# Kernel tuning notes

Measured on AMD Instinct MI355X. Metric: run time of the kernel, lower is better.

## Reference

```python
import jax, jax.numpy as jnp
import numpy as np

NODE, EDGE, GLOB, HID = 128, 64, 64, 32
E, B = 500000, 1024
IN = 2 * NODE + EDGE + GLOB  # 384


def setup_inputs() -> dict:
    key = jax.random.key(0)
    ks = jax.random.split(key, 9)
    src = jax.random.normal(ks[0], (E, NODE), dtype=jnp.float32)
    dest = jax.random.normal(ks[1], (E, NODE), dtype=jnp.float32)
    edge_attr = jax.random.normal(ks[2], (E, EDGE), dtype=jnp.float32)
    u = jax.random.normal(ks[3], (B, GLOB), dtype=jnp.float32)
    batch = jnp.sort(jax.random.randint(ks[4], (E,), 0, B, dtype=jnp.int64))
    # MLP params (Linear stores weight [out,in]; we keep [in,out] for x@W)
    s1 = 1.0 / np.sqrt(IN)
    s2 = 1.0 / np.sqrt(HID)
    W1 = jax.random.uniform(ks[5], (IN, HID), jnp.float32, -s1, s1)
    b1 = jax.random.uniform(ks[6], (HID,), jnp.float32, -s1, s1)
    W2 = jax.random.uniform(ks[7], (HID, EDGE), jnp.float32, -s2, s2)
    b2 = jax.random.uniform(ks[8], (EDGE,), jnp.float32, -s2, s2)
    return {"src": src, "dest": dest, "edge_attr": edge_attr, "u": u,
            "batch": batch, "W1": W1, "b1": b1, "W2": W2, "b2": b2}


def reference(src, dest, edge_attr, u, batch, W1, b1, W2, b2):
    # gather per-edge global features, concat, 2-layer MLP with SELU
    x = jnp.concatenate([src, dest, edge_attr, u[batch]], axis=1)  # [E, 384]
    h = jax.nn.selu(x @ W1 + b1)  # [E, 32]
    return h @ W2 + b2            # [E, 64]
```

## Files before the change

### kernel.cpp

```cpp
#include <hip/hip_runtime.h>
#include <hip/hip_bf16.h>

#define N_E    500000
#define D_NODE 128
#define D_EDGE 64
#define D_GLOB 64
#define NTILES (N_E / 16)

typedef __attribute__((ext_vector_type(8))) short s16x8;
typedef __attribute__((ext_vector_type(4))) float fx4;

__device__ __forceinline__ unsigned short f2bf(float x) {
  union { __hip_bfloat16 h; unsigned short u; } cv;
  cv.h = __float2bfloat16(x);
  return cv.u;
}

__device__ __forceinline__ s16x8 pack8(fx4 a, fx4 b) {
  s16x8 r;
  r[0] = (short)f2bf(a[0]); r[1] = (short)f2bf(a[1]);
  r[2] = (short)f2bf(a[2]); r[3] = (short)f2bf(a[3]);
  r[4] = (short)f2bf(b[0]); r[5] = (short)f2bf(b[1]);
  r[6] = (short)f2bf(b[2]); r[7] = (short)f2bf(b[3]);
  return r;
}

__global__ __launch_bounds__(256) void edge_mlp_kernel(
    const float* __restrict__ src, const float* __restrict__ dst,
    const float* __restrict__ ea,  const float* __restrict__ u,
    const int*   __restrict__ batch,
    const float* __restrict__ W1,  const float* __restrict__ b1,
    const float* __restrict__ W2,  const float* __restrict__ b2,
    float* __restrict__ out)
{
  __shared__ unsigned short w1t[32][392];
  __shared__ unsigned short w2t[64][40];
  __shared__ float b1s[32];
  __shared__ float b2s[64];
  __shared__ unsigned short hstage[4][16][40];

  const int tid = threadIdx.x;

  for (int i = tid; i < 384 * 32; i += 256) {
    int k = i >> 5, n = i & 31;
    w1t[n][k] = f2bf(W1[i]);
  }
  for (int i = tid; i < 32 * 64; i += 256) {
    int k = i >> 6, n = i & 63;
    w2t[n][k] = f2bf(W2[i]);
  }
  if (tid < 32) b1s[tid] = b1[tid];
  if (tid < 64) b2s[tid] = b2[tid];
  __syncthreads();

  const int wave = tid >> 6;
  const int lane = tid & 63;
  const int c  = lane & 15;
  const int r4 = lane >> 4;
  const int r8 = r4 * 8;
  unsigned short (*hl)[40] = hstage[wave];

  const int gwave  = blockIdx.x * 4 + wave;
  const int nwaves = gridDim.x * 4;

  const float lam = 1.0507009873554805f;
  const float la  = 1.7580993408473766f;

  for (int tile = gwave; tile < NTILES; tile += nwaves) {
    const int e0   = tile * 16;
    const int arow = e0 + c;

    const float* sp  = src + (size_t)arow * D_NODE + r8;
    const float* dp  = dst + (size_t)arow * D_NODE + r8;
    const float* epp = ea  + (size_t)arow * D_EDGE + r8;
    const int    bt  = batch[arow];
    const float* up  = u   + (size_t)bt * D_GLOB + r8;

    const float* bases[12] = { sp, sp + 32, sp + 64, sp + 96,
                               dp, dp + 32, dp + 64, dp + 96,
                               epp, epp + 32, up, up + 32 };
    fx4 raw[24];
#pragma unroll
    for (int i = 0; i < 12; ++i) {
      const fx4* q = (const fx4*)bases[i];
      raw[2 * i]     = q[0];
      raw[2 * i + 1] = q[1];
    }

    s16x8 af[12];
#pragma unroll
    for (int i = 0; i < 12; ++i) af[i] = pack8(raw[2 * i], raw[2 * i + 1]);

    fx4 acc0 = {0.f, 0.f, 0.f, 0.f};
    fx4 acc1 = {0.f, 0.f, 0.f, 0.f};
#pragma unroll
    for (int kk = 0; kk < 12; ++kk) {
      s16x8 bf0 = *(const s16x8*)&w1t[c][kk * 32 + r8];
      s16x8 bf1 = *(const s16x8*)&w1t[c + 16][kk * 32 + r8];
      acc0 = __builtin_amdgcn_mfma_f32_16x16x32_bf16(af[kk], bf0, acc0, 0, 0, 0);
      acc1 = __builtin_amdgcn_mfma_f32_16x16x32_bf16(af[kk], bf1, acc1, 0, 0, 0);
    }

#pragma unroll
    for (int t = 0; t < 2; ++t) {
      const float bb = b1s[c + 16 * t];
      fx4 a = t ? acc1 : acc0;
#pragma unroll
      for (int r = 0; r < 4; ++r) {
        float v = a[r] + bb;
        v = v > 0.f ? lam * v : la * (__expf(v) - 1.f);
        hl[r4 * 4 + r][c + 16 * t] = f2bf(v);
      }
    }

    s16x8 a2 = *(const s16x8*)&hl[c][r8];
    fx4 o0, o1, o2, o3;
    { float bb = b2s[c];      o0 = (fx4){bb, bb, bb, bb}; }
    { float bb = b2s[c + 16]; o1 = (fx4){bb, bb, bb, bb}; }
    { float bb = b2s[c + 32]; o2 = (fx4){bb, bb, bb, bb}; }
    { float bb = b2s[c + 48]; o3 = (fx4){bb, bb, bb, bb}; }
    o0 = __builtin_amdgcn_mfma_f32_16x16x32_bf16(a2, *(const s16x8*)&w2t[c][r8],      o0, 0, 0, 0);
    o1 = __builtin_amdgcn_mfma_f32_16x16x32_bf16(a2, *(const s16x8*)&w2t[c + 16][r8], o1, 0, 0, 0);
    o2 = __builtin_amdgcn_mfma_f32_16x16x32_bf16(a2, *(const s16x8*)&w2t[c + 32][r8], o2, 0, 0, 0);
    o3 = __builtin_amdgcn_mfma_f32_16x16x32_bf16(a2, *(const s16x8*)&w2t[c + 48][r8], o3, 0, 0, 0);

#pragma unroll
    for (int r = 0; r < 4; ++r) {
      float* op = out + (size_t)(e0 + r4 * 4 + r) * 64 + c;
      op[0]  = o0[r];
      op[16] = o1[r];
      op[32] = o2[r];
      op[48] = o3[r];
    }
  }
}

extern "C" void kernel_launch(void* const* d_in, const int* in_sizes, int n_in,
                              void* d_out, int out_size, void* d_ws, size_t ws_size,
                              hipStream_t stream) {
  const float* src   = (const float*)d_in[0];
  const float* dst   = (const float*)d_in[1];
  const float* ea    = (const float*)d_in[2];
  const float* u     = (const float*)d_in[3];
  const int*   batch = (const int*)d_in[4];
  const float* W1    = (const float*)d_in[5];
  const float* b1    = (const float*)d_in[6];
  const float* W2    = (const float*)d_in[7];
  const float* b2    = (const float*)d_in[8];
  float* out = (float*)d_out;

  hipLaunchKernelGGL(edge_mlp_kernel, dim3(2048), dim3(256), 0, stream,
                     src, dst, ea, u, batch, W1, b1, W2, b2, out);
}
```

Before: 151.4 us.

## Coalesce edge-feature loads via LDS staging and assign contiguous tiles per wave

Each wave now reads its 16-row tile of src, dst and edge_attr as fully contiguous 16-byte-per-lane chunks. It converts them to bf16 and writes them into a per-wave LDS buffer, then reads back the MFMA A-fragments from LDS. Before, each lane made strided per-row loads. The hidden staging buffer is aliased onto the same LDS region. The grid changes from a fixed 2048 blocks with a grid-stride loop to one block per 16 tiles, so each wave handles 4 consecutive tiles. This adds about 50KB of LDS per block, which may reduce occupancy, and adds LDS write/read traffic in exchange for better global-load coalescing.

```diff
diff --git a/kernel.cpp b/kernel.cpp
--- a/kernel.cpp
+++ b/kernel.cpp
@@ -6,9 +6,11 @@
 #define D_EDGE 64
 #define D_GLOB 64
 #define NTILES (N_E / 16)
+#define TPW    4
 
 typedef __attribute__((ext_vector_type(8))) short s16x8;
 typedef __attribute__((ext_vector_type(4))) float fx4;
+typedef __attribute__((ext_vector_type(2))) unsigned int u32x2;
 
 __device__ __forceinline__ unsigned short f2bf(float x) {
   union { __hip_bfloat16 h; unsigned short u; } cv;
@@ -16,12 +18,10 @@
   return cv.u;
 }
 
-__device__ __forceinline__ s16x8 pack8(fx4 a, fx4 b) {
-  s16x8 r;
-  r[0] = (short)f2bf(a[0]); r[1] = (short)f2bf(a[1]);
-  r[2] = (short)f2bf(a[2]); r[3] = (short)f2bf(a[3]);
-  r[4] = (short)f2bf(b[0]); r[5] = (short)f2bf(b[1]);
-  r[6] = (short)f2bf(b[2]); r[7] = (short)f2bf(b[3]);
+__device__ __forceinline__ u32x2 cvt4(fx4 v) {
+  u32x2 r;
+  r[0] = (unsigned)f2bf(v[0]) | ((unsigned)f2bf(v[1]) << 16);
+  r[1] = (unsigned)f2bf(v[2]) | ((unsigned)f2bf(v[3]) << 16);
   return r;
 }
 
@@ -35,9 +35,9 @@
 {
   __shared__ unsigned short w1t[32][392];
   __shared__ unsigned short w2t[64][40];
+  __shared__ unsigned short Xs[4][16][392];
   __shared__ float b1s[32];
   __shared__ float b2s[64];
-  __shared__ unsigned short hstage[4][16][40];
 
   const int tid = threadIdx.x;
 
@@ -58,38 +58,66 @@
   const int c  = lane & 15;
   const int r4 = lane >> 4;
   const int r8 = r4 * 8;
-  unsigned short (*hl)[40] = hstage[wave];
+  const int l5  = lane >> 5, l31 = lane & 31;
+  const int l4  = lane >> 4, l15 = lane & 15;
 
-  const int gwave  = blockIdx.x * 4 + wave;
-  const int nwaves = gridDim.x * 4;
+  unsigned short (*X)[392] = Xs[wave];
+  unsigned short (*hl)[40] = (unsigned short (*)[40])&Xs[wave][0][0];
+
+  const int gw = blockIdx.x * 4 + wave;
+  const int t0 = gw * TPW;
+  const int t1 = (t0 + TPW < NTILES) ? t0 + TPW : NTILES;
+  if (t0 >= NTILES) return;
 
   const float lam = 1.0507009873554805f;
   const float la  = 1.7580993408473766f;
 
-  for (int tile = gwave; tile < NTILES; tile += nwaves) {
-    const int e0   = tile * 16;
-    const int arow = e0 + c;
+  for (int tile = t0; tile < t1; ++tile) {
+    const int e0 = tile * 16;
 
-    const float* sp  = src + (size_t)arow * D_NODE + r8;
-    const float* dp  = dst + (size_t)arow * D_NODE + r8;
-    const float* epp = ea  + (size_t)arow * D_EDGE + r8;
-    const int    bt  = batch[arow];
-    const float* up  = u   + (size_t)bt * D_GLOB + r8;
+    const char* sb = (const char*)(src + (size_t)e0 * D_NODE);
+    const char* db = (const char*)(dst + (size_t)e0 * D_NODE);
+    const char* eb = (const char*)(ea  + (size_t)e0 * D_EDGE);
 
-    const float* bases[12] = { sp, sp + 32, sp + 64, sp + 96,
-                               dp, dp + 32, dp + 64, dp + 96,
-                               epp, epp + 32, up, up + 32 };
-    fx4 raw[24];
+    fx4 vs[8], vd[8], ve[4], vu[4];
 #pragma unroll
-    for (int i = 0; i < 12; ++i) {
-      const fx4* q = (const fx4*)bases[i];
-      raw[2 * i]     = q[0];
-      raw[2 * i + 1] = q[1];
+    for (int i = 0; i < 8; ++i) vs[i] = *(const fx4*)(sb + i * 1024 + lane * 16);
+#pragma unroll
+    for (int i = 0; i < 8; ++i) vd[i] = *(const fx4*)(db + i * 1024 + lane * 16);
+#pragma unroll
+    for (int i = 0; i < 4; ++i) ve[i] = *(const fx4*)(eb + i * 1024 + lane * 16);
+    int bts[4];
+#pragma unroll
+    for (int i = 0; i < 4; ++i) bts[i] = batch[e0 + i * 4 + l4];
+#pragma unroll
+    for (int i = 0; i < 4; ++i)
+      vu[i] = *(const fx4*)((const char*)u + (size_t)bts[i] * 256 + l15 * 16);
+
+#pragma unroll
+    for (int i = 0; i < 8; ++i) {
+      u32x2 p = cvt4(vs[i]);
+      *(u32x2*)((char*)&X[2 * i + l5][0] + l31 * 8) = p;
+    }
+#pragma unroll
+    for (int i = 0; i < 8; ++i) {
+      u32x2 p = cvt4(vd[i]);
+      *(u32x2*)((char*)&X[2 * i + l5][128] + l31 * 8) = p;
+    }
+#pragma unroll
+    for (int i = 0; i < 4; ++i) {
+      u32x2 p = cvt4(ve[i]);
+      *(u32x2*)((char*)&X[4 * i + l4][256] + l15 * 8) = p;
+    }
+#pragma unroll
+    for (int i = 0; i < 4; ++i) {
+      u32x2 p = cvt4(vu[i]);
+      *(u32x2*)((char*)&X[4 * i + l4][320] + l15 * 8) = p;
     }
 
     s16x8 af[12];
 #pragma unroll
-    for (int i = 0; i < 12; ++i) af[i] = pack8(raw[2 * i], raw[2 * i + 1]);
+    for (int kk = 0; kk < 12; ++kk)
+      af[kk] = *(const s16x8*)&X[c][kk * 32 + r8];
 
     fx4 acc0 = {0.f, 0.f, 0.f, 0.f};
     fx4 acc1 = {0.f, 0.f, 0.f, 0.f};
@@ -149,6 +177,8 @@
   const float* b2    = (const float*)d_in[8];
   float* out = (float*)d_out;
 
-  hipLaunchKernelGGL(edge_mlp_kernel, dim3(2048), dim3(256), 0, stream,
+  const int nwaves  = (NTILES + TPW - 1) / TPW;
+  const int nblocks = (nwaves + 3) / 4;
+  hipLaunchKernelGGL(edge_mlp_kernel, dim3(nblocks), dim3(256), 0, stream,
                      src, dst, ea, u, batch, W1, b1, W2, b2, out);
 }
```

New measurement: 183.5 us. 21.2% more time.

## Double-buffer edge tiles into LDS via async global_load_lds with register-resident weights

Applied to the files above, without the earlier changes.

Each wave now owns a contiguous range of tiles and prefetches the next tile's src/dst/edge/u rows straight into a swizzled LDS buffer with global_load_lds while it computes the current tile. The MLP weights and biases are held in registers per lane, so the per-block LDS weight staging and its syncthreads go away. The grid shrinks to 256 blocks of 3 waves with roughly 48KB of LDS per wave, which means one block per CU and low occupancy. Memory latency is hidden by the explicit pipeline instead of by many waves in flight, and the heavy register and LDS use per wave is the risk.

```diff
diff --git a/kernel.cpp b/kernel.cpp
--- a/kernel.cpp
+++ b/kernel.cpp
@@ -2,13 +2,18 @@
 #include <hip/hip_bf16.h>
 
 #define N_E    500000
-#define D_NODE 128
-#define D_EDGE 64
-#define D_GLOB 64
 #define NTILES (N_E / 16)
+#define NWAVES 768
+#define BUF_BYTES 24576
+#define WAVE_LDS  (2 * BUF_BYTES)
+#define HL_BASE   (3 * WAVE_LDS)
+#define SMEM_TOTAL (HL_BASE + 3 * 1280)
 
 typedef __attribute__((ext_vector_type(8))) short s16x8;
 typedef __attribute__((ext_vector_type(4))) float fx4;
+
+typedef __attribute__((address_space(1))) const void glb_void;
+typedef __attribute__((address_space(3))) void lds_void;
 
 __device__ __forceinline__ unsigned short f2bf(float x) {
   union { __hip_bfloat16 h; unsigned short u; } cv;
@@ -25,7 +30,48 @@
   return r;
 }
 
-__global__ __launch_bounds__(256) void edge_mlp_kernel(
+__device__ __forceinline__ void gl2lds16(const void* g, void* l) {
+  __builtin_amdgcn_global_load_lds((glb_void*)g, (lds_void*)l, 16, 0, 0);
+}
+
+__device__ __forceinline__ void stage_tile(
+    int e0, int lane, int bvals,
+    const float* __restrict__ src, const float* __restrict__ dst,
+    const float* __restrict__ ea,  const float* __restrict__ u,
+    char* bx)
+{
+#pragma unroll
+  for (int i = 0; i < 8; ++i) {
+    int V = i * 64 + lane;
+    int row = V >> 5, w = V & 31;
+    int wsw = w ^ (row & 7);
+    gl2lds16((const char*)src + (size_t)(e0 + row) * 512 + wsw * 16, bx + i * 1024);
+  }
+#pragma unroll
+  for (int i = 0; i < 8; ++i) {
+    int V = i * 64 + lane;
+    int row = V >> 5, w = V & 31;
+    int wsw = w ^ (row & 7);
+    gl2lds16((const char*)dst + (size_t)(e0 + row) * 512 + wsw * 16, bx + 8192 + i * 1024);
+  }
+#pragma unroll
+  for (int i = 0; i < 4; ++i) {
+    int V = i * 64 + lane;
+    int row = V >> 4, w = V & 15;
+    int wsw = w ^ (row & 7);
+    gl2lds16((const char*)ea + (size_t)(e0 + row) * 256 + wsw * 16, bx + 16384 + i * 1024);
+  }
+#pragma unroll
+  for (int i = 0; i < 4; ++i) {
+    int row = i * 4 + (lane >> 4);
+    int bt  = __shfl(bvals, row);
+    int w   = lane & 15;
+    int wsw = w ^ (row & 7);
+    gl2lds16((const char*)u + (size_t)bt * 256 + wsw * 16, bx + 20480 + i * 1024);
+  }
+}
+
+__global__ __launch_bounds__(192, 1) void edge_mlp_kernel(
     const float* __restrict__ src, const float* __restrict__ dst,
     const float* __restrict__ ea,  const float* __restrict__ u,
     const int*   __restrict__ batch,
@@ -33,97 +79,124 @@
     const float* __restrict__ W2,  const float* __restrict__ b2,
     float* __restrict__ out)
 {
-  __shared__ unsigned short w1t[32][392];
-  __shared__ unsigned short w2t[64][40];
-  __shared__ float b1s[32];
-  __shared__ float b2s[64];
-  __shared__ unsigned short hstage[4][16][40];
-
-  const int tid = threadIdx.x;
-
-  for (int i = tid; i < 384 * 32; i += 256) {
-    int k = i >> 5, n = i & 31;
-    w1t[n][k] = f2bf(W1[i]);
-  }
-  for (int i = tid; i < 32 * 64; i += 256) {
-    int k = i >> 6, n = i & 63;
-    w2t[n][k] = f2bf(W2[i]);
-  }
-  if (tid < 32) b1s[tid] = b1[tid];
-  if (tid < 64) b2s[tid] = b2[tid];
-  __syncthreads();
-
+  __shared__ __align__(1024) char smem[SMEM_TOTAL];
+
+  const int tid  = threadIdx.x;
   const int wave = tid >> 6;
   const int lane = tid & 63;
   const int c  = lane & 15;
   const int r4 = lane >> 4;
   const int r8 = r4 * 8;
-  unsigned short (*hl)[40] = hstage[wave];
-
-  const int gwave  = blockIdx.x * 4 + wave;
-  const int nwaves = gridDim.x * 4;
+
+  s16x8 wf0[12], wf1[12];
+#pragma unroll
+  for (int kk = 0; kk < 12; ++kk)
+#pragma unroll
+    for (int j = 0; j < 8; ++j) {
+      wf0[kk][j] = (short)f2bf(W1[(kk * 32 + r8 + j) * 32 + c]);
+      wf1[kk][j] = (short)f2bf(W1[(kk * 32 + r8 + j) * 32 + c + 16]);
+    }
+  s16x8 wf2[4];
+#pragma unroll
+  for (int t = 0; t < 4; ++t)
+#pragma unroll
+    for (int j = 0; j < 8; ++j)
+      wf2[t][j] = (short)f2bf(W2[(r8 + j) * 64 + c + 16 * t]);
+  const float bb10 = b1[c], bb11 = b1[c + 16];
+  float bb2v[4];
+#pragma unroll
+  for (int t = 0; t < 4; ++t) bb2v[t] = b2[c + 16 * t];
+
+  const int gw = blockIdx.x * 3 + wave;
+  const int q = NTILES / NWAVES, rem = NTILES % NWAVES;
+  const int t0 = gw * q + (gw < rem ? gw : rem);
+  const int t1 = t0 + q + (gw < rem ? 1 : 0);
+
+  char* x0 = smem + wave * WAVE_LDS;
+  char* x1 = x0 + BUF_BYTES;
+  unsigned short (*hl)[40] = (unsigned short (*)[40])(smem + HL_BASE + wave * 1280);
 
   const float lam = 1.0507009873554805f;
   const float la  = 1.7580993408473766f;
 
-  for (int tile = gwave; tile < NTILES; tile += nwaves) {
-    const int e0   = tile * 16;
-    const int arow = e0 + c;
-
-    const float* sp  = src + (size_t)arow * D_NODE + r8;
-    const float* dp  = dst + (size_t)arow * D_NODE + r8;
-    const float* epp = ea  + (size_t)arow * D_EDGE + r8;
-    const int    bt  = batch[arow];
-    const float* up  = u   + (size_t)bt * D_GLOB + r8;
-
-    const float* bases[12] = { sp, sp + 32, sp + 64, sp + 96,
-                               dp, dp + 32, dp + 64, dp + 96,
-                               epp, epp + 32, up, up + 32 };
-    fx4 raw[24];
-#pragma unroll
-    for (int i = 0; i < 12; ++i) {
-      const fx4* q = (const fx4*)bases[i];
-      raw[2 * i]     = q[0];
-      raw[2 * i + 1] = q[1];
-    }
+  int bv_nxt = batch[t0 * 16 + c];
+  stage_tile(t0 * 16, lane, bv_nxt, src, dst, ea, u, x0);
+  {
+    const int tn = (t0 + 1 < t1) ? t0 + 1 : t1 - 1;
+    bv_nxt = batch[tn * 16 + c];
+  }
+
+  char* cur = x0;
+  char* nxt = x1;
+
+  for (int t = t0; t < t1; ++t) {
+    const int tn = (t + 1 < t1) ? t + 1 : t1 - 1;
+
+    __builtin_amdgcn_sched_barrier(0);
+    asm volatile("s_waitcnt lgkmcnt(0)" ::: "memory");
+    stage_tile(tn * 16, lane, bv_nxt, src, dst, ea, u, nxt);
+    __builtin_amdgcn_sched_barrier(0);
+    asm volatile("s_waitcnt vmcnt(24)" ::: "memory");
+    __builtin_amdgcn_sched_barrier(0);
+
+    const int tn2 = (t + 2 < t1) ? t + 2 : t1 - 1;
+    int bv_new = batch[tn2 * 16 + c];
 
     s16x8 af[12];
 #pragma unroll
-    for (int i = 0; i < 12; ++i) af[i] = pack8(raw[2 * i], raw[2 * i + 1]);
+    for (int kk = 0; kk < 4; ++kk) {
+      int u0 = (kk * 8 + r4 * 2)     ^ (c & 7);
+      int u1 = (kk * 8 + r4 * 2 + 1) ^ (c & 7);
+      fx4 lo = *(const fx4*)(cur + c * 512 + u0 * 16);
+      fx4 hi = *(const fx4*)(cur + c * 512 + u1 * 16);
+      af[kk] = pack8(lo, hi);
+      lo = *(const fx4*)(cur + 8192 + c * 512 + u0 * 16);
+      hi = *(const fx4*)(cur + 8192 + c * 512 + u1 * 16);
+      af[4 + kk] = pack8(lo, hi);
+    }
+#pragma unroll
+    for (int m = 0; m < 2; ++m) {
+      int u0 = (m * 8 + r4 * 2)     ^ (c & 7);
+      int u1 = (m * 8 + r4 * 2 + 1) ^ (c & 7);
+      fx4 lo = *(const fx4*)(cur + 16384 + c * 256 + u0 * 16);
+      fx4 hi = *(const fx4*)(cur + 16384 + c * 256 + u1 * 16);
+      af[8 + m] = pack8(lo, hi);
+      lo = *(const fx4*)(cur + 20480 + c * 256 + u0 * 16);
+      hi = *(const fx4*)(cur + 20480 + c * 256 + u1 * 16);
+      af[10 + m] = pack8(lo, hi);
+    }
 
     fx4 acc0 = {0.f, 0.f, 0.f, 0.f};
     fx4 acc1 = {0.f, 0.f, 0.f, 0.f};
 #pragma unroll
     for (int kk = 0; kk < 12; ++kk) {
-      s16x8 bf0 = *(const s16x8*)&w1t[c][kk * 32 + r8];
-      s16x8 bf1 = *(const s16x8*)&w1t[c + 16][kk * 32 + r8];
-      acc0 = __builtin_amdgcn_mfma_f32_16x16x32_bf16(af[kk], bf0, acc0, 0, 0, 0);
-      acc1 = __builtin_amdgcn_mfma_f32_16x16x32_bf16(af[kk], bf1, acc1, 0, 0, 0);
-    }
-
-#pragma unroll
-    for (int t = 0; t < 2; ++t) {
-      const float bb = b1s[c + 16 * t];
-      fx4 a = t ? acc1 : acc0;
+      acc0 = __builtin_amdgcn_mfma_f32_16x16x32_bf16(af[kk], wf0[kk], acc0, 0, 0, 0);
+      acc1 = __builtin_amdgcn_mfma_f32_16x16x32_bf16(af[kk], wf1[kk], acc1, 0, 0, 0);
+    }
+
+#pragma unroll
+    for (int tt = 0; tt < 2; ++tt) {
+      const float bb = tt ? bb11 : bb10;
+      fx4 a = tt ? acc1 : acc0;
 #pragma unroll
       for (int r = 0; r < 4; ++r) {
         float v = a[r] + bb;
         v = v > 0.f ? lam * v : la * (__expf(v) - 1.f);
-        hl[r4 * 4 + r][c + 16 * t] = f2bf(v);
+        hl[r4 * 4 + r][c + 16 * tt] = f2bf(v);
       }
     }
 
     s16x8 a2 = *(const s16x8*)&hl[c][r8];
-    fx4 o0, o1, o2, o3;
-    { float bb = b2s[c];      o0 = (fx4){bb, bb, bb, bb}; }
-    { float bb = b2s[c + 16]; o1 = (fx4){bb, bb, bb, bb}; }
-    { float bb = b2s[c + 32]; o2 = (fx4){bb, bb, bb, bb}; }
-    { float bb = b2s[c + 48]; o3 = (fx4){bb, bb, bb, bb}; }
-    o0 = __builtin_amdgcn_mfma_f32_16x16x32_bf16(a2, *(const s16x8*)&w2t[c][r8],      o0, 0, 0, 0);
-    o1 = __builtin_amdgcn_mfma_f32_16x16x32_bf16(a2, *(const s16x8*)&w2t[c + 16][r8], o1, 0, 0, 0);
-    o2 = __builtin_amdgcn_mfma_f32_16x16x32_bf16(a2, *(const s16x8*)&w2t[c + 32][r8], o2, 0, 0, 0);
-    o3 = __builtin_amdgcn_mfma_f32_16x16x32_bf16(a2, *(const s16x8*)&w2t[c + 48][r8], o3, 0, 0, 0);
-
+    fx4 o0 = {bb2v[0], bb2v[0], bb2v[0], bb2v[0]};
+    fx4 o1 = {bb2v[1], bb2v[1], bb2v[1], bb2v[1]};
+    fx4 o2 = {bb2v[2], bb2v[2], bb2v[2], bb2v[2]};
+    fx4 o3 = {bb2v[3], bb2v[3], bb2v[3], bb2v[3]};
+    o0 = __builtin_amdgcn_mfma_f32_16x16x32_bf16(a2, wf2[0], o0, 0, 0, 0);
+    o1 = __builtin_amdgcn_mfma_f32_16x16x32_bf16(a2, wf2[1], o1, 0, 0, 0);
+    o2 = __builtin_amdgcn_mfma_f32_16x16x32_bf16(a2, wf2[2], o2, 0, 0, 0);
+    o3 = __builtin_amdgcn_mfma_f32_16x16x32_bf16(a2, wf2[3], o3, 0, 0, 0);
+
+    const int e0 = t * 16;
 #pragma unroll
     for (int r = 0; r < 4; ++r) {
       float* op = out + (size_t)(e0 + r4 * 4 + r) * 64 + c;
@@ -132,6 +205,9 @@
       op[32] = o2[r];
       op[48] = o3[r];
     }
+
+    bv_nxt = bv_new;
+    char* tmp = cur; cur = nxt; nxt = tmp;
   }
 }
 
@@ -149,6 +225,6 @@
   const float* b2    = (const float*)d_in[8];
   float* out = (float*)d_out;
 
-  hipLaunchKernelGGL(edge_mlp_kernel, dim3(2048), dim3(256), 0, stream,
+  hipLaunchKernelGGL(edge_mlp_kernel, dim3(256), dim3(192), 0, stream,
                      src, dst, ea, u, batch, W1, b1, W2, b2, out);
 }
```

Measured after the change: 168.4 us. 1.11x slower.
